# Kernel optimization log

Hardware: AMD Instinct MI355X
Metric: run time of the kernel (lower is better)

## Reference

```python
import jax, jax.numpy as jnp
import numpy as np

LSTM_H = 128
HID = 64
EMB = 64
GRU2_H = 50
B, T = 2048, 200
NODE_NUM = 50000


def _lstm_dir(x_proj, w_hh, reverse):
    # x_proj: (T, B, 4H) = x @ W_ih^T + b_ih + b_hh, precomputed
    Bn = x_proj.shape[1]
    H = w_hh.shape[1]
    h0 = jnp.zeros((Bn, H), x_proj.dtype)

    def step(carry, xp):
        h, c = carry
        gates = xp + h @ w_hh.T
        i, f, g, o = jnp.split(gates, 4, axis=-1)  # torch gate order i,f,g,o
        i = jax.nn.sigmoid(i); f = jax.nn.sigmoid(f)
        g = jnp.tanh(g); o = jax.nn.sigmoid(o)
        c = f * c + i * g
        h = o * jnp.tanh(c)
        return (h, c), h

    (hT, _), hs = jax.lax.scan(step, (h0, h0), x_proj, reverse=reverse)
    return hs, hT  # hs: (T,B,H) time-aligned; hT: final hidden of this direction


def _bilstm(x, wih_f, whh_f, b_f, wih_b, whh_b, b_b):
    # x: (B,T,I) batch_first -> scan over time
    xt = jnp.swapaxes(x, 0, 1)  # (T,B,I)
    hs_f, h_f = _lstm_dir(xt @ wih_f.T + b_f, whh_f, False)
    hs_b, h_b = _lstm_dir(xt @ wih_b.T + b_b, whh_b, True)
    out = jnp.concatenate([hs_f, hs_b], axis=-1)  # (T,B,2H)
    return jnp.swapaxes(out, 0, 1), jnp.stack([h_f, h_b])  # (B,T,2H), (2,B,H)


def _gru(x, h, wih, whh, bih, bhh):
    gi = x @ wih.T + bih
    gh = h @ whh.T + bhh
    ir, iz, inn = jnp.split(gi, 3, axis=-1)  # torch gate order r,z,n
    hr, hz, hn = jnp.split(gh, 3, axis=-1)
    r = jax.nn.sigmoid(ir + hr)
    z = jax.nn.sigmoid(iz + hz)
    n = jnp.tanh(inn + r * hn)
    return (1.0 - z) * n + z * h


def setup_inputs() -> dict:
    key = jax.random.key(0)
    ks = iter(jax.random.split(key, 40))
    s = 0.05
    d = {}
    d['node_data'] = jax.random.randint(next(ks), (B, 2), 0, NODE_NUM)
    d['edge_data'] = jax.random.uniform(next(ks), (B, T, 1), jnp.float32)
    d['emb'] = jax.random.normal(next(ks), (NODE_NUM, EMB), jnp.float32) * s
    # LSTM 1: input 1, hidden 128, bidirectional (b = b_ih + b_hh fused)
    d['l1_wih_f'] = jax.random.normal(next(ks), (4 * LSTM_H, 1), jnp.float32) * s
    d['l1_whh_f'] = jax.random.normal(next(ks), (4 * LSTM_H, LSTM_H), jnp.float32) * s
    d['l1_b_f'] = jax.random.normal(next(ks), (4 * LSTM_H,), jnp.float32) * s
    d['l1_wih_b'] = jax.random.normal(next(ks), (4 * LSTM_H, 1), jnp.float32) * s
    d['l1_whh_b'] = jax.random.normal(next(ks), (4 * LSTM_H, LSTM_H), jnp.float32) * s
    d['l1_b_b'] = jax.random.normal(next(ks), (4 * LSTM_H,), jnp.float32) * s
    # LSTM 2: input 256, hidden 128, bidirectional
    d['l2_wih_f'] = jax.random.normal(next(ks), (4 * LSTM_H, 2 * LSTM_H), jnp.float32) * s
    d['l2_whh_f'] = jax.random.normal(next(ks), (4 * LSTM_H, LSTM_H), jnp.float32) * s
    d['l2_b_f'] = jax.random.normal(next(ks), (4 * LSTM_H,), jnp.float32) * s
    d['l2_wih_b'] = jax.random.normal(next(ks), (4 * LSTM_H, 2 * LSTM_H), jnp.float32) * s
    d['l2_whh_b'] = jax.random.normal(next(ks), (4 * LSTM_H, LSTM_H), jnp.float32) * s
    d['l2_b_b'] = jax.random.normal(next(ks), (4 * LSTM_H,), jnp.float32) * s
    # encoder FCs
    d['fc1_w'] = jax.random.normal(next(ks), (2 * LSTM_H, 2 * LSTM_H), jnp.float32) * s
    d['fc1_b'] = jnp.zeros((2 * LSTM_H,), jnp.float32)
    d['fc2_w'] = jax.random.normal(next(ks), (HID, 2 * LSTM_H), jnp.float32) * s
    d['fc2_b'] = jnp.zeros((HID,), jnp.float32)
    # GRUCell 1: input 1, hidden HID+EMB=128
    G1 = HID + EMB
    d['g1_wih'] = jax.random.normal(next(ks), (3 * G1, 1), jnp.float32) * s
    d['g1_whh'] = jax.random.normal(next(ks), (3 * G1, G1), jnp.float32) * s
    d['g1_bih'] = jax.random.normal(next(ks), (3 * G1,), jnp.float32) * s
    d['g1_bhh'] = jax.random.normal(next(ks), (3 * G1,), jnp.float32) * s
    # GRUCell 2: input 128, hidden 50
    d['g2_wih'] = jax.random.normal(next(ks), (3 * GRU2_H, G1), jnp.float32) * s
    d['g2_whh'] = jax.random.normal(next(ks), (3 * GRU2_H, GRU2_H), jnp.float32) * s
    d['g2_bih'] = jax.random.normal(next(ks), (3 * GRU2_H,), jnp.float32) * s
    d['g2_bhh'] = jax.random.normal(next(ks), (3 * GRU2_H,), jnp.float32) * s
    # decoder FC: 50 -> 1
    d['dec_w'] = jax.random.normal(next(ks), (1, GRU2_H), jnp.float32) * s
    d['dec_b'] = jnp.zeros((1,), jnp.float32)
    return d


def reference(node_data, edge_data, emb,
              l1_wih_f, l1_whh_f, l1_b_f, l1_wih_b, l1_whh_b, l1_b_b,
              l2_wih_f, l2_whh_f, l2_b_f, l2_wih_b, l2_whh_b, l2_b_b,
              fc1_w, fc1_b, fc2_w, fc2_b,
              g1_wih, g1_whh, g1_bih, g1_bhh,
              g2_wih, g2_whh, g2_bih, g2_bhh,
              dec_w, dec_b):
    # ---- encoder ----
    node_embs = emb[node_data]                      # (B,2,EMB)
    node_emb = node_embs.mean(axis=1)               # (head+tail)/2
    h1_out, hn1 = _bilstm(edge_data, l1_wih_f, l1_whh_f, l1_b_f,
                          l1_wih_b, l1_whh_b, l1_b_b)
    _, hn2 = _bilstm(h1_out, l2_wih_f, l2_whh_f, l2_b_f,
                     l2_wih_b, l2_whh_b, l2_b_b)
    # faithful to original: view (2,B,128) -> (-1, 256) row-major (interleaves dir/batch)
    hidden_lstm = hn1.reshape(-1, 2 * LSTM_H) + hn2.reshape(-1, 2 * LSTM_H)
    h_fc1 = jax.nn.sigmoid(hidden_lstm @ fc1_w.T + fc1_b)  # dropout = identity (eval)
    temp_emb = jax.nn.sigmoid(h_fc1 @ fc2_w.T + fc2_b)
    hidden = jnp.concatenate([temp_emb, node_emb], axis=1)  # (B, HID+EMB)
    # ---- decoder: sequential GRU unroll as a scan ----
    Bn, max_len = edge_data.shape[0], edge_data.shape[1]
    h2_0 = jnp.zeros((Bn, GRU2_H), edge_data.dtype)

    def dstep(carry, _):
        res, h1, h2 = carry
        h1n = _gru(res, h1, g1_wih, g1_whh, g1_bih, g1_bhh)
        h2n = _gru(h1n, h2, g2_wih, g2_whh, g2_bih, g2_bhh)
        resn = jax.nn.sigmoid(h2n @ dec_w.T + dec_b)        # (B,1)
        return (resn, h1n, h2n), resn

    init = (edge_data[:, -1], hidden, h2_0)
    _, results = jax.lax.scan(dstep, init, None, length=max_len)
    return jnp.swapaxes(results, 0, 1)  # (B, max_len, 1)
```

## Files before the change

kernel.cpp:

```cpp
#include <hip/hip_runtime.h>
#include <stdint.h>

typedef short bf16x8 __attribute__((ext_vector_type(8)));
typedef float f32x4  __attribute__((ext_vector_type(4)));
typedef unsigned short u16;

#define NBATCH 2048
#define NT 200

#define MFMA_AG(accv, av, wfrag) \
  asm("v_mfma_f32_16x16x32_bf16 %0, %1, %2, %0" : "+v"(accv) : "v"(av), "a"(wfrag))
#define SEED_A(x) asm volatile("" : "+a"(x))
#define BAR() asm volatile("s_waitcnt lgkmcnt(0)\n\ts_barrier" ::: "memory")

#define OFF_HN1   209715200ull
#define OFF_HN2   211812352ull
#define OFF_ZC    213909504ull

__device__ __forceinline__ short f2bf(float f){
  union { float f; uint32_t u; } v; v.f = f;
  uint32_t u = v.u;
  u += 0x7fffu + ((u >> 16) & 1u);
  return (short)(u >> 16);
}
__device__ __forceinline__ float sigm(float x){
  return __builtin_amdgcn_rcpf(1.0f + __expf(-x));
}
__device__ __forceinline__ float tanh_(float x){
  return fmaf(-2.0f, __builtin_amdgcn_rcpf(1.0f + __expf(2.0f * x)), 1.0f);
}

__global__ void prep_l12(const float* __restrict__ l1hf, const float* __restrict__ l1hb,
                         const float* __restrict__ l2wf, const float* __restrict__ l2hf,
                         const float* __restrict__ l2wb, const float* __restrict__ l2hb,
                         u16* __restrict__ wl1, u16* __restrict__ wl2)
{
  int idx = blockIdx.x * 256 + threadIdx.x;
  if (idx < 16384){
    int tid = idx & 511, r = idx >> 9;
    int kt = r & 3, g = (r >> 2) & 3, d = r >> 4;
    const float* whh = d ? l1hb : l1hf;
    int wv = tid >> 6, ln = tid & 63, lr = ln & 15, lk = ln >> 4;
    int n = g * 128 + wv * 16 + lr;
    const float* s = whh + (size_t)n * 128 + kt * 32 + lk * 8;
    bf16x8 w;
#pragma unroll
    for (int i = 0; i < 8; ++i) w[i] = f2bf(s[i]);
    *(bf16x8*)(wl1 + (size_t)idx * 8) = w;
  } else {
    int j = idx - 16384;
    int tid = j & 511, r = j >> 9;
    int kt = r % 12, rg = r / 12;
    int g = rg & 3, d = rg >> 2;
    const float* wih = d ? l2wb : l2wf;
    const float* whh = d ? l2hb : l2hf;
    int wv = tid >> 6, ln = tid & 63, lr = ln & 15, lk = ln >> 4;
    int n = g * 128 + wv * 16 + lr;
    const float* s = (kt < 8) ? (wih + (size_t)n * 256 + kt * 32 + lk * 8)
                              : (whh + (size_t)n * 128 + (kt - 8) * 32 + lk * 8);
    bf16x8 w;
#pragma unroll
    for (int i = 0; i < 8; ++i) w[i] = f2bf(s[i]);
    *(bf16x8*)(wl2 + (size_t)j * 8) = w;
  }
}

__global__ void prep2(const float* __restrict__ g1whh, const float* __restrict__ g2wih,
                      const float* __restrict__ g2whh,
                      const float* __restrict__ fc1w, const float* __restrict__ fc2w,
                      const int* __restrict__ nd, const float* __restrict__ emb,
                      u16* __restrict__ wd1, u16* __restrict__ wd2i, u16* __restrict__ wd2h,
                      float* __restrict__ fc1wT, float* __restrict__ fc2wT,
                      float* __restrict__ ne)
{
  int idx = blockIdx.x * 256 + threadIdx.x;
  if (idx < 6144){
    int tid = idx & 511, r = idx >> 9;
    int kt = r & 3, g = r >> 2;
    int wv = tid >> 6, ln = tid & 63, lr = ln & 15, lk = ln >> 4;
    int n = g * 128 + wv * 16 + lr;
    const float* s = g1whh + (size_t)n * 128 + kt * 32 + lk * 8;
    bf16x8 w;
#pragma unroll
    for (int i = 0; i < 8; ++i) w[i] = f2bf(s[i]);
    *(bf16x8*)(wd1 + (size_t)idx * 8) = w;
  } else if (idx < 9216){
    int j = idx - 6144;
    int tid = j & 255, r = j >> 8;
    int kt = r & 3, g = r >> 2;
    int wv = tid >> 6, ln = tid & 63, lr = ln & 15, lk = ln >> 4;
    int jj = wv * 16 + lr;
    bf16x8 w;
#pragma unroll
    for (int i = 0; i < 8; ++i){
      int k = kt * 32 + lk * 8 + i;
      w[i] = (jj < 50) ? f2bf(g2wih[(size_t)(g * 50 + jj) * 128 + k]) : (short)0;
    }
    *(bf16x8*)(wd2i + (size_t)j * 8) = w;
  } else if (idx < 10752){
    int j = idx - 9216;
    int tid = j & 255, r = j >> 8;
    int kt = r & 1, g = r >> 1;
    int wv = tid >> 6, ln = tid & 63, lr = ln & 15, lk = ln >> 4;
    int jj = wv * 16 + lr;
    bf16x8 w;
#pragma unroll
    for (int i = 0; i < 8; ++i){
      int k = kt * 32 + lk * 8 + i;
      w[i] = (jj < 50 && k < 50) ? f2bf(g2whh[(size_t)(g * 50 + jj) * 50 + k]) : (short)0;
    }
    *(bf16x8*)(wd2h + (size_t)j * 8) = w;
  } else if (idx < 10752 + 65536){
    int j = idx - 10752;
    int n = j & 255, k = j >> 8;
    fc1wT[(size_t)k * 256 + n] = fc1w[(size_t)n * 256 + k];
  } else if (idx < 10752 + 81920){
    int j = idx - 10752 - 65536;
    int m = j & 63, k = j >> 6;
    fc2wT[(size_t)k * 64 + m] = fc2w[(size_t)m * 256 + k];
  } else {
    int t = idx - 92672;
    int row = t >> 6, e = t & 63;
    int i0 = nd[row * 2], i1 = nd[row * 2 + 1];
    ne[t] = 0.5f * (emb[(size_t)i0 * 64 + e] + emb[(size_t)i1 * 64 + e]);
  }
}

#define L1_KT(kt) { \
  int off = lr * 256 + (((kt) * 64 + lk * 16) ^ ((lr & 7) << 4)); \
  bf16x8 a = *(const bf16x8*)(hb + off); \
  MFMA_AG(acc[0], a, W[0][kt]); MFMA_AG(acc[1], a, W[1][kt]); \
  MFMA_AG(acc[2], a, W[2][kt]); MFMA_AG(acc[3], a, W[3][kt]); }

__global__ __launch_bounds__(512) __attribute__((amdgpu_waves_per_eu(2, 2))) void k_l1(
    const float* __restrict__ edge, const u16* __restrict__ wl1,
    const float* __restrict__ wih_f, const float* __restrict__ b_f,
    const float* __restrict__ wih_b, const float* __restrict__ b_b,
    u16* __restrict__ h1out, float* __restrict__ hn1)
{
  const int bid = blockIdx.x;
  const int dir = bid >> 7;
  const int b0  = (bid & 127) * 16;
  const float* wih = dir ? wih_b : wih_f;
  const float* bia = dir ? b_b  : b_f;

  const int tid = threadIdx.x;
  const int wv  = tid >> 6;
  const int ln  = tid & 63;
  const int lr  = ln & 15;
  const int lk  = ln >> 4;

  __shared__ __align__(16) short hbf[2][16 * 128];
  __shared__ float xall[16][NT];

  bf16x8 W[4][4];
  const u16* wb = wl1 + (size_t)dir * 16 * 512 * 8;
  float wv_[4], bv_[4];
#pragma unroll
  for (int g = 0; g < 4; ++g){
    int n = g * 128 + wv * 16 + lr;
    wv_[g] = wih[n];
    bv_[g] = bia[n];
#pragma unroll
    for (int kt = 0; kt < 4; ++kt){
      W[g][kt] = *(const bf16x8*)(wb + ((size_t)(g * 4 + kt) * 512 + tid) * 8);
      SEED_A(W[g][kt]);
    }
  }
  for (int i = tid; i < 16 * 128; i += 512) hbf[0][i] = 0;
  for (int i = tid; i < 16 * NT; i += 512){
    int r = i / NT, t = i - r * NT;
    xall[r][t] = edge[(b0 + r) * NT + t];
  }
  float cst[4] = {0.f, 0.f, 0.f, 0.f};
  float hseg[4] = {0.f, 0.f, 0.f, 0.f};
  __syncthreads();

  for (int s = 0; s < NT; ++s){
    const int p = s & 1;
    const int t = dir ? (NT - 1 - s) : s;

    const char* hb = (const char*)hbf + p * (16 * 256);
    f32x4 acc[4];
    float xq[4];
#pragma unroll
    for (int q = 0; q < 4; ++q) xq[q] = xall[lk * 4 + q][t];
#pragma unroll
    for (int g = 0; g < 4; ++g){
#pragma unroll
      for (int q = 0; q < 4; ++q) acc[g][q] = fmaf(xq[q], wv_[g], bv_[g]);
    }
    if (wv & 1){ L1_KT(2) L1_KT(3) L1_KT(0) L1_KT(1) }
    else       { L1_KT(0) L1_KT(1) L1_KT(2) L1_KT(3) }
    char* hbw = (char*)hbf + (p ^ 1) * (16 * 256);
#pragma unroll
    for (int q = 0; q < 4; ++q){
      float iv = sigm(acc[0][q]);
      float fv = sigm(acc[1][q]);
      float gv = tanh_(acc[2][q]);
      float ov = sigm(acc[3][q]);
      cst[q] = fv * cst[q] + iv * gv;
      hseg[q] = ov * tanh_(cst[q]);
      short hv = f2bf(hseg[q]);
      int r = lk * 4 + q, j = wv * 16 + lr;
      h1out[((size_t)t * NBATCH + b0 + r) * 256 + dir * 128 + j] = (u16)hv;
      *(short*)(hbw + r * 256 + ((2 * j) ^ ((r & 7) << 4))) = hv;
    }
    BAR();
  }
#pragma unroll
  for (int q = 0; q < 4; ++q)
    hn1[((size_t)dir * NBATCH + b0 + lk * 4 + q) * 128 + wv * 16 + lr] = hseg[q];
}

#define L2_LDSKT(kt) { \
  int off = lr * 768 + (((kt) * 64 + lk * 16) ^ ((lr & 7) << 4)); \
  bf16x8 a = *(const bf16x8*)(ab + off); \
  bf16x8 w0 = *(const bf16x8*)&wlds[((size_t)(0 * 4 + (kt)) * 512 + tid) * 8]; \
  acc[0] = __builtin_amdgcn_mfma_f32_16x16x32_bf16(a, w0, acc[0], 0, 0, 0); \
  bf16x8 w1 = *(const bf16x8*)&wlds[((size_t)(1 * 4 + (kt)) * 512 + tid) * 8]; \
  acc[1] = __builtin_amdgcn_mfma_f32_16x16x32_bf16(a, w1, acc[1], 0, 0, 0); \
  bf16x8 w2 = *(const bf16x8*)&wlds[((size_t)(2 * 4 + (kt)) * 512 + tid) * 8]; \
  acc[2] = __builtin_amdgcn_mfma_f32_16x16x32_bf16(a, w2, acc[2], 0, 0, 0); \
  bf16x8 w3 = *(const bf16x8*)&wlds[((size_t)(3 * 4 + (kt)) * 512 + tid) * 8]; \
  acc[3] = __builtin_amdgcn_mfma_f32_16x16x32_bf16(a, w3, acc[3], 0, 0, 0); }

#define L2_AGKT(k8) { \
  int off = lr * 768 + (((4 + (k8)) * 64 + lk * 16) ^ ((lr & 7) << 4)); \
  bf16x8 a = *(const bf16x8*)(ab + off); \
  MFMA_AG(acc[0], a, Wa[0][k8]); MFMA_AG(acc[1], a, Wa[1][k8]); \
  MFMA_AG(acc[2], a, Wa[2][k8]); MFMA_AG(acc[3], a, Wa[3][k8]); }

__global__ __launch_bounds__(512) __attribute__((amdgpu_waves_per_eu(2, 2))) void k_l2(
    const u16* __restrict__ h1out, const u16* __restrict__ wl2,
    const float* __restrict__ b_f, const float* __restrict__ b_b,
    float* __restrict__ hn2)
{
  const int bid = blockIdx.x;
  const int dir = bid >> 7;
  const int b0  = (bid & 127) * 16;
  const float* bia = dir ? b_b : b_f;

  const int tid = threadIdx.x;
  const int wv  = tid >> 6;
  const int ln  = tid & 63;
  const int lr  = ln & 15;
  const int lk  = ln >> 4;

  __shared__ __align__(16) short wlds[16 * 512 * 8];
  __shared__ __align__(16) short Ab[2][16 * 384];

  const u16* wb = wl2 + (size_t)dir * 48 * 512 * 8;
#pragma unroll
  for (int f = 0; f < 16; ++f){
    int g = f >> 2, kt = f & 3;
    *(bf16x8*)&wlds[((size_t)f * 512 + tid) * 8] =
        *(const bf16x8*)(wb + ((size_t)(g * 12 + kt) * 512 + tid) * 8);
  }
  bf16x8 Wa[4][8];
  float bv_[4];
#pragma unroll
  for (int g = 0; g < 4; ++g){
    bv_[g] = bia[g * 128 + wv * 16 + lr];
#pragma unroll
    for (int k8 = 0; k8 < 8; ++k8){
      Wa[g][k8] = *(const bf16x8*)(wb + ((size_t)(g * 12 + 4 + k8) * 512 + tid) * 8);
      SEED_A(Wa[g][k8]);
    }
  }
  for (int i = tid; i < 16 * 128; i += 512){
    int r = i >> 7, j = i & 127;
    *(short*)((char*)Ab + r * 768 + ((512 + 2 * j) ^ ((r & 7) << 4))) = 0;
  }
  const int sr = tid >> 5, sg = tid & 31;
  {
    int t0 = dir ? NT - 1 : 0;
    bf16x8 v = *(const bf16x8*)(h1out + ((size_t)t0 * NBATCH + b0 + sr) * 256 + sg * 8);
    *(bf16x8*)((char*)Ab + sr * 768 + ((sg * 16) ^ ((sr & 7) << 4))) = v;
  }
  float cst[4] = {0.f, 0.f, 0.f, 0.f};
  float hseg[4] = {0.f, 0.f, 0.f, 0.f};
  __syncthreads();

  for (int s = 0; s < NT; ++s){
    const int p = s & 1;
    const int t = dir ? (NT - 1 - s) : s;
    const int tn = dir ? (t > 0 ? t - 1 : 0) : (t < NT - 1 ? t + 1 : NT - 1);
    bf16x8 xr = *(const bf16x8*)(h1out + ((size_t)tn * NBATCH + b0 + sr) * 256 + sg * 8);

    const char* ab = (const char*)Ab + p * (16 * 768);
    f32x4 acc[4];
#pragma unroll
    for (int g = 0; g < 4; ++g){
#pragma unroll
      for (int q = 0; q < 4; ++q) acc[g][q] = bv_[g];
    }
    if (wv & 1){
      L2_AGKT(0) L2_AGKT(1) L2_AGKT(2) L2_AGKT(3)
      L2_AGKT(4) L2_AGKT(5) L2_AGKT(6) L2_AGKT(7)
      L2_LDSKT(0) L2_LDSKT(1) L2_LDSKT(2) L2_LDSKT(3)
    } else {
      L2_LDSKT(0) L2_LDSKT(1) L2_LDSKT(2) L2_LDSKT(3)
      L2_AGKT(0) L2_AGKT(1) L2_AGKT(2) L2_AGKT(3)
      L2_AGKT(4) L2_AGKT(5) L2_AGKT(6) L2_AGKT(7)
    }
    char* abw = (char*)Ab + (p ^ 1) * (16 * 768);
#pragma unroll
    for (int q = 0; q < 4; ++q){
      float iv = sigm(acc[0][q]);
      float fv = sigm(acc[1][q]);
      float gv = tanh_(acc[2][q]);
      float ov = sigm(acc[3][q]);
      cst[q] = fv * cst[q] + iv * gv;
      hseg[q] = ov * tanh_(cst[q]);
      int r = lk * 4 + q, j = wv * 16 + lr;
      *(short*)(abw + r * 768 + ((512 + 2 * j) ^ ((r & 7) << 4))) = f2bf(hseg[q]);
    }
    *(bf16x8*)(abw + sr * 768 + ((sg * 16) ^ ((sr & 7) << 4))) = xr;
    BAR();
  }
#pragma unroll
  for (int q = 0; q < 4; ++q)
    hn2[((size_t)dir * NBATCH + b0 + lk * 4 + q) * 128 + wv * 16 + lr] = hseg[q];
}

__global__ __launch_bounds__(256) void k_fc(
    const float* __restrict__ hn1, const float* __restrict__ hn2,
    const float* __restrict__ fc1wT, const float* __restrict__ fc1b,
    const float* __restrict__ fc2wT, const float* __restrict__ fc2b,
    const float* __restrict__ ne, float* __restrict__ hidden)
{
  __shared__ float X[16][256];
  __shared__ float Y[16][256];
  const int b0 = blockIdx.x * 16;
  const int tid = threadIdx.x;
  for (int i = tid; i < 16 * 256; i += 256){
    int rr = i >> 8, cc = i & 255;
    size_t o = (size_t)(b0 + rr) * 256 + cc;
    X[rr][cc] = hn1[o] + hn2[o];
  }
  __syncthreads();
  {
    const int n = tid;
    float a[16];
#pragma unroll
    for (int r = 0; r < 16; ++r) a[r] = fc1b[n];
    for (int k = 0; k < 256; ++k){
      float w = fc1wT[(size_t)k * 256 + n];
#pragma unroll
      for (int r = 0; r < 16; ++r) a[r] = fmaf(X[r][k], w, a[r]);
    }
#pragma unroll
    for (int r = 0; r < 16; ++r) Y[r][n] = sigm(a[r]);
  }
  __syncthreads();
  {
    const int m = tid & 63, rg = tid >> 6;
    float a2[4];
#pragma unroll
    for (int q = 0; q < 4; ++q) a2[q] = fc2b[m];
    for (int k = 0; k < 256; ++k){
      float w = fc2wT[(size_t)k * 64 + m];
#pragma unroll
      for (int q = 0; q < 4; ++q) a2[q] = fmaf(Y[rg * 4 + q][k], w, a2[q]);
    }
#pragma unroll
    for (int q = 0; q < 4; ++q)
      hidden[(size_t)(b0 + rg * 4 + q) * 128 + m] = sigm(a2[q]);
  }
  for (int i = tid; i < 16 * 64; i += 256){
    int rr = i >> 6, e = i & 63;
    hidden[(size_t)(b0 + rr) * 128 + 64 + e] = ne[(size_t)(b0 + rr) * 64 + e];
  }
}

#define D1_KT(kt) { \
  int off = lr * 256 + (((kt) * 64 + lk * 16) ^ ((lr & 7) << 4)); \
  bf16x8 a = *(const bf16x8*)(h1r + off); \
  MFMA_AG(ar, a, W1[0][kt]); MFMA_AG(az, a, W1[1][kt]); MFMA_AG(an, a, W1[2][kt]); }

#define D2_KT(kt) { \
  int off = lr * 256 + (((kt) * 64 + lk * 16) ^ ((lr & 7) << 4)); \
  bf16x8 a = *(const bf16x8*)(h1n + off); \
  MFMA_AG(gi0, a, Wi2[0][kt]); MFMA_AG(gi1, a, Wi2[1][kt]); MFMA_AG(gi2v, a, Wi2[2][kt]); }

__global__ __launch_bounds__(512) __attribute__((amdgpu_waves_per_eu(2, 2))) void k_dec(
    const float* __restrict__ edge, const float* __restrict__ hidden,
    const float* __restrict__ g1wih, const float* __restrict__ g1bih,
    const float* __restrict__ g1bhh, const u16* __restrict__ wd1,
    const float* __restrict__ g2bih, const float* __restrict__ g2bhh,
    const u16* __restrict__ wd2i, const u16* __restrict__ wd2h,
    const float* __restrict__ decw, const float* __restrict__ decb,
    float* __restrict__ out)
{
  const int b0 = blockIdx.x * 16;
  const int tid = threadIdx.x;
  const int wv  = tid >> 6;
  const int ln  = tid & 63;
  const int lr  = ln & 15;
  const int lk  = ln >> 4;

  __shared__ __align__(16) short h1bf[2][16 * 128];
  __shared__ __align__(16) short h2bf[2][16 * 64];
  __shared__ float part[2][4][16];

  bf16x8 W1[3][4];
  float wih1v[3], bih1v[3], bhh1v[3];
#pragma unroll
  for (int g = 0; g < 3; ++g){
    int n = g * 128 + wv * 16 + lr;
    wih1v[g] = g1wih[n];
    bih1v[g] = g1bih[n];
    bhh1v[g] = g1bhh[n];
#pragma unroll
    for (int kt = 0; kt < 4; ++kt){
      W1[g][kt] = *(const bf16x8*)(wd1 + ((size_t)(g * 4 + kt) * 512 + tid) * 8);
      SEED_A(W1[g][kt]);
    }
  }
  bf16x8 Wi2[3][4], Wh2[3][2];
  float bih2v[3] = {0,0,0}, bhh2v[3] = {0,0,0}, dwv = 0.f;
  const int jj = wv * 16 + lr;
  if (wv < 4){
    bool nv_ = (jj < 50);
    dwv = nv_ ? decw[jj] : 0.f;
#pragma unroll
    for (int g = 0; g < 3; ++g){
      bih2v[g] = nv_ ? g2bih[g * 50 + jj] : 0.f;
      bhh2v[g] = nv_ ? g2bhh[g * 50 + jj] : 0.f;
#pragma unroll
      for (int kt = 0; kt < 4; ++kt){
        Wi2[g][kt] = *(const bf16x8*)(wd2i + ((size_t)(g * 4 + kt) * 256 + tid) * 8);
        SEED_A(Wi2[g][kt]);
      }
#pragma unroll
      for (int kt = 0; kt < 2; ++kt){
        Wh2[g][kt] = *(const bf16x8*)(wd2h + ((size_t)(g * 2 + kt) * 256 + tid) * 8);
        SEED_A(Wh2[g][kt]);
      }
    }
  }
  float h1s[4], h2s[4] = {0.f, 0.f, 0.f, 0.f}, e4[4];
#pragma unroll
  for (int q = 0; q < 4; ++q){
    h1s[q] = hidden[(size_t)(b0 + lk * 4 + q) * 128 + wv * 16 + lr];
    int r = lk * 4 + q, j = wv * 16 + lr;
    *(short*)((char*)h1bf + r * 256 + ((2 * j) ^ ((r & 7) << 4))) = f2bf(h1s[q]);
    e4[q] = edge[(b0 + r) * NT + NT - 1];
  }
  for (int i = tid; i < 16 * 64; i += 512) h2bf[0][i] = 0;
  const float db = decb[0];
  __syncthreads();

  for (int s = 0; s < NT; ++s){
    const int p = s & 1;
    float res_q[4];
    if (s == 0){
#pragma unroll
      for (int q = 0; q < 4; ++q) res_q[q] = e4[q];
    } else {
#pragma unroll
      for (int q = 0; q < 4; ++q){
        int row = lk * 4 + q;
        float sum = part[p][0][row] + part[p][1][row] + part[p][2][row] + part[p][3][row] + db;
        res_q[q] = sigm(sum);
        if (wv == 0 && lr == 0) out[(size_t)(b0 + row) * NT + (s - 1)] = res_q[q];
      }
    }
    const char* h1r = (const char*)h1bf + p * (16 * 256);
    f32x4 ar, az, an;
#pragma unroll
    for (int q = 0; q < 4; ++q){ ar[q] = bhh1v[0]; az[q] = bhh1v[1]; an[q] = bhh1v[2]; }
    if (wv & 1){ D1_KT(2) D1_KT(3) D1_KT(0) D1_KT(1) }
    else       { D1_KT(0) D1_KT(1) D1_KT(2) D1_KT(3) }
    char* h1w = (char*)h1bf + (p ^ 1) * (16 * 256);
#pragma unroll
    for (int q = 0; q < 4; ++q){
      float res = res_q[q];
      float rv = sigm(fmaf(res, wih1v[0], bih1v[0]) + ar[q]);
      float zv = sigm(fmaf(res, wih1v[1], bih1v[1]) + az[q]);
      float nv = tanh_(fmaf(res, wih1v[2], bih1v[2]) + rv * an[q]);
      h1s[q] = (1.f - zv) * nv + zv * h1s[q];
      int r = lk * 4 + q, j = wv * 16 + lr;
      *(short*)(h1w + r * 256 + ((2 * j) ^ ((r & 7) << 4))) = f2bf(h1s[q]);
    }
    BAR();
    if (wv < 4){
      f32x4 gi0, gi1, gi2v, gh0, gh1, gh2v;
#pragma unroll
      for (int q = 0; q < 4; ++q){
        gi0[q] = bih2v[0]; gi1[q] = bih2v[1]; gi2v[q] = bih2v[2];
        gh0[q] = bhh2v[0]; gh1[q] = bhh2v[1]; gh2v[q] = bhh2v[2];
      }
      const char* h1n = (const char*)h1bf + (p ^ 1) * (16 * 256);
      if (wv & 1){ D2_KT(2) D2_KT(3) D2_KT(0) D2_KT(1) }
      else       { D2_KT(0) D2_KT(1) D2_KT(2) D2_KT(3) }
      const char* h2r = (const char*)h2bf + p * (16 * 128);
#pragma unroll
      for (int kt = 0; kt < 2; ++kt){
        int off = lr * 128 + ((kt * 64 + lk * 16) ^ ((lr & 7) << 4));
        bf16x8 a = *(const bf16x8*)(h2r + off);
        MFMA_AG(gh0,  a, Wh2[0][kt]);
        MFMA_AG(gh1,  a, Wh2[1][kt]);
        MFMA_AG(gh2v, a, Wh2[2][kt]);
      }
      char* h2w = (char*)h2bf + (p ^ 1) * (16 * 128);
      float pd[4];
#pragma unroll
      for (int q = 0; q < 4; ++q){
        float r2 = sigm(gi0[q] + gh0[q]);
        float z2 = sigm(gi1[q] + gh1[q]);
        float n2 = tanh_(gi2v[q] + r2 * gh2v[q]);
        h2s[q] = (1.f - z2) * n2 + z2 * h2s[q];
        pd[q] = h2s[q] * dwv;
        int r = lk * 4 + q, j = wv * 16 + lr;
        *(short*)(h2w + r * 128 + ((2 * j) ^ ((r & 7) << 4))) = f2bf(h2s[q]);
      }
#pragma unroll
      for (int m = 1; m < 16; m <<= 1){
#pragma unroll
        for (int q = 0; q < 4; ++q) pd[q] += __shfl_xor(pd[q], m);
      }
      if (lr == 0){
#pragma unroll
        for (int q = 0; q < 4; ++q) part[p ^ 1][wv][lk * 4 + q] = pd[q];
      }
    }
    BAR();
  }
  if (wv == 0 && lr == 0){
#pragma unroll
    for (int q = 0; q < 4; ++q){
      int row = lk * 4 + q;
      float sum = part[0][0][row] + part[0][1][row] + part[0][2][row] + part[0][3][row] + db;
      out[(size_t)(b0 + row) * NT + (NT - 1)] = sigm(sum);
    }
  }
}

extern "C" void kernel_launch(void* const* d_in, const int* in_sizes, int n_in,
                              void* d_out, int out_size, void* d_ws, size_t ws_size,
                              hipStream_t stream)
{
  (void)in_sizes; (void)n_in; (void)out_size; (void)ws_size;
  const int*   nd    = (const int*)  d_in[0];
  const float* edge  = (const float*)d_in[1];
  const float* emb   = (const float*)d_in[2];
  const float* l1wf  = (const float*)d_in[3];
  const float* l1hf  = (const float*)d_in[4];
  const float* l1bf  = (const float*)d_in[5];
  const float* l1wb  = (const float*)d_in[6];
  const float* l1hb  = (const float*)d_in[7];
  const float* l1bb  = (const float*)d_in[8];
  const float* l2wf  = (const float*)d_in[9];
  const float* l2hf  = (const float*)d_in[10];
  const float* l2bf  = (const float*)d_in[11];
  const float* l2wb  = (const float*)d_in[12];
  const float* l2hb  = (const float*)d_in[13];
  const float* l2bb  = (const float*)d_in[14];
  const float* fc1w  = (const float*)d_in[15];
  const float* fc1b  = (const float*)d_in[16];
  const float* fc2w  = (const float*)d_in[17];
  const float* fc2b  = (const float*)d_in[18];
  const float* g1wih = (const float*)d_in[19];
  const float* g1whh = (const float*)d_in[20];
  const float* g1bih = (const float*)d_in[21];
  const float* g1bhh = (const float*)d_in[22];
  const float* g2wih = (const float*)d_in[23];
  const float* g2whh = (const float*)d_in[24];
  const float* g2bih = (const float*)d_in[25];
  const float* g2bhh = (const float*)d_in[26];
  const float* decw  = (const float*)d_in[27];
  const float* decb  = (const float*)d_in[28];

  char* ws = (char*)d_ws;
  u16*   h1out  = (u16*)ws;
  u16*   wd1    = (u16*)ws;
  u16*   wd2i   = (u16*)(ws + 98304);
  u16*   wd2h   = (u16*)(ws + 147456);
  float* fc1wT  = (float*)(ws + 262144);
  float* fc2wT  = (float*)(ws + 524288);
  float* hn1    = (float*)(ws + OFF_HN1);
  float* hn2    = (float*)(ws + OFF_HN2);
  u16*   wl2    = (u16*)(ws + OFF_ZC);
  u16*   wl1    = (u16*)(ws + OFF_ZC + 786432);
  float* ne     = (float*)(ws + OFF_ZC);
  float* hidden = (float*)(ws + OFF_ZC + 524288);

  prep_l12<<<dim3(256), dim3(256), 0, stream>>>(l1hf, l1hb, l2wf, l2hf, l2wb, l2hb, wl1, wl2);
  k_l1<<<dim3(256), dim3(512), 0, stream>>>(edge, wl1, l1wf, l1bf, l1wb, l1bb, h1out, hn1);
  k_l2<<<dim3(256), dim3(512), 0, stream>>>(h1out, wl2, l2bf, l2bb, hn2);
  prep2<<<dim3(874), dim3(256), 0, stream>>>(g1whh, g2wih, g2whh, fc1w, fc2w, nd, emb,
                                             wd1, wd2i, wd2h, fc1wT, fc2wT, ne);
  k_fc<<<dim3(128), dim3(256), 0, stream>>>(hn1, hn2, fc1wT, fc1b, fc2wT, fc2b, ne, hidden);
  k_dec<<<dim3(128), dim3(512), 0, stream>>>(edge, hidden, g1wih, g1bih, g1bhh, wd1,
                                             g2bih, g2bhh, wd2i, wd2h, decw, decb,
                                             (float*)d_out);
}
```

Before: 1.046 ms.

## Split LSTM1 into 8-row blocks and software-pipeline LSTM2 input projection

Layer-1 LSTM now runs 512 blocks of 256 threads, each handling 8 batch rows with every wave computing two 16-column tiles per gate. The MFMA uses only half of its 16 rows; the other half are duplicates. This spreads the serial recurrence over more CUs at the price of doing the MFMA work twice. Layer-2 now keeps the input-projection buffer separate from the hidden-state buffer, and computes the input part for the next step before the current step's gate nonlinearities, so that part falls outside the serial h dependency chain. The register-held weights move to the Wx and Wh halves, and the split of weights between registers and LDS changes with them.

```diff
diff --git a/kernel.cpp b/kernel.cpp
--- a/kernel.cpp
+++ b/kernel.cpp
@@ -37,11 +37,11 @@
 {
   int idx = blockIdx.x * 256 + threadIdx.x;
   if (idx < 16384){
-    int tid = idx & 511, r = idx >> 9;
-    int kt = r & 3, g = (r >> 2) & 3, d = r >> 4;
+    int tid = idx & 255, r = idx >> 8;
+    int kt = r & 3, u = (r >> 2) & 1, g = (r >> 3) & 3, d = r >> 5;
     const float* whh = d ? l1hb : l1hf;
     int wv = tid >> 6, ln = tid & 63, lr = ln & 15, lk = ln >> 4;
-    int n = g * 128 + wv * 16 + lr;
+    int n = g * 128 + wv * 32 + u * 16 + lr;
     const float* s = whh + (size_t)n * 128 + kt * 32 + lk * 8;
     bf16x8 w;
 #pragma unroll
@@ -126,21 +126,15 @@
   }
 }
 
-#define L1_KT(kt) { \
-  int off = lr * 256 + (((kt) * 64 + lk * 16) ^ ((lr & 7) << 4)); \
-  bf16x8 a = *(const bf16x8*)(hb + off); \
-  MFMA_AG(acc[0], a, W[0][kt]); MFMA_AG(acc[1], a, W[1][kt]); \
-  MFMA_AG(acc[2], a, W[2][kt]); MFMA_AG(acc[3], a, W[3][kt]); }
-
-__global__ __launch_bounds__(512) __attribute__((amdgpu_waves_per_eu(2, 2))) void k_l1(
+__global__ __launch_bounds__(256) __attribute__((amdgpu_waves_per_eu(2, 2))) void k_l1(
     const float* __restrict__ edge, const u16* __restrict__ wl1,
     const float* __restrict__ wih_f, const float* __restrict__ b_f,
     const float* __restrict__ wih_b, const float* __restrict__ b_b,
     u16* __restrict__ h1out, float* __restrict__ hn1)
 {
   const int bid = blockIdx.x;
-  const int dir = bid >> 7;
-  const int b0  = (bid & 127) * 16;
+  const int dir = bid >> 8;
+  const int b0  = (bid & 255) * 8;
   const float* wih = dir ? wih_b : wih_f;
   const float* bia = dir ? b_b  : b_f;
 
@@ -151,29 +145,31 @@
   const int lk  = ln >> 4;
 
   __shared__ __align__(16) short hbf[2][16 * 128];
-  __shared__ float xall[16][NT];
-
-  bf16x8 W[4][4];
-  const u16* wb = wl1 + (size_t)dir * 16 * 512 * 8;
-  float wv_[4], bv_[4];
-#pragma unroll
-  for (int g = 0; g < 4; ++g){
-    int n = g * 128 + wv * 16 + lr;
-    wv_[g] = wih[n];
-    bv_[g] = bia[n];
-#pragma unroll
-    for (int kt = 0; kt < 4; ++kt){
-      W[g][kt] = *(const bf16x8*)(wb + ((size_t)(g * 4 + kt) * 512 + tid) * 8);
-      SEED_A(W[g][kt]);
-    }
-  }
-  for (int i = tid; i < 16 * 128; i += 512) hbf[0][i] = 0;
-  for (int i = tid; i < 16 * NT; i += 512){
+  __shared__ float xall[8][NT];
+
+  bf16x8 W[4][2][4];
+  const u16* wb = wl1 + (size_t)dir * 32 * 256 * 8;
+  float wv_[4][2], bv_[4][2];
+#pragma unroll
+  for (int g = 0; g < 4; ++g)
+#pragma unroll
+    for (int u = 0; u < 2; ++u){
+      int n = g * 128 + wv * 32 + u * 16 + lr;
+      wv_[g][u] = wih[n];
+      bv_[g][u] = bia[n];
+#pragma unroll
+      for (int kt = 0; kt < 4; ++kt){
+        W[g][u][kt] = *(const bf16x8*)(wb + ((size_t)((g * 8 + u * 4 + kt)) * 256 + tid) * 8);
+        SEED_A(W[g][u][kt]);
+      }
+    }
+  for (int i = tid; i < 16 * 128; i += 256) hbf[0][i] = 0;
+  for (int i = tid; i < 8 * NT; i += 256){
     int r = i / NT, t = i - r * NT;
     xall[r][t] = edge[(b0 + r) * NT + t];
   }
-  float cst[4] = {0.f, 0.f, 0.f, 0.f};
-  float hseg[4] = {0.f, 0.f, 0.f, 0.f};
+  float cst[2][4] = {{0,0,0,0},{0,0,0,0}};
+  float hseg[2][4] = {{0,0,0,0},{0,0,0,0}};
   __syncthreads();
 
   for (int s = 0; s < NT; ++s){
@@ -181,55 +177,53 @@
     const int t = dir ? (NT - 1 - s) : s;
 
     const char* hb = (const char*)hbf + p * (16 * 256);
-    f32x4 acc[4];
+    f32x4 acc[4][2];
     float xq[4];
 #pragma unroll
-    for (int q = 0; q < 4; ++q) xq[q] = xall[lk * 4 + q][t];
-#pragma unroll
-    for (int g = 0; g < 4; ++g){
-#pragma unroll
-      for (int q = 0; q < 4; ++q) acc[g][q] = fmaf(xq[q], wv_[g], bv_[g]);
-    }
-    if (wv & 1){ L1_KT(2) L1_KT(3) L1_KT(0) L1_KT(1) }
-    else       { L1_KT(0) L1_KT(1) L1_KT(2) L1_KT(3) }
+    for (int q = 0; q < 4; ++q) xq[q] = xall[(lk * 4 + q) & 7][t];
+#pragma unroll
+    for (int g = 0; g < 4; ++g)
+#pragma unroll
+      for (int u = 0; u < 2; ++u)
+#pragma unroll
+        for (int q = 0; q < 4; ++q) acc[g][u][q] = fmaf(xq[q], wv_[g][u], bv_[g][u]);
+#pragma unroll
+    for (int kt = 0; kt < 4; ++kt){
+      int off = lr * 256 + ((kt * 64 + lk * 16) ^ ((lr & 7) << 4));
+      bf16x8 a = *(const bf16x8*)(hb + off);
+#pragma unroll
+      for (int g = 0; g < 4; ++g)
+#pragma unroll
+        for (int u = 0; u < 2; ++u) MFMA_AG(acc[g][u], a, W[g][u][kt]);
+    }
     char* hbw = (char*)hbf + (p ^ 1) * (16 * 256);
 #pragma unroll
+    for (int u = 0; u < 2; ++u)
+#pragma unroll
+      for (int q = 0; q < 4; ++q){
+        float iv = sigm(acc[0][u][q]);
+        float fv = sigm(acc[1][u][q]);
+        float gv = tanh_(acc[2][u][q]);
+        float ov = sigm(acc[3][u][q]);
+        cst[u][q] = fv * cst[u][q] + iv * gv;
+        hseg[u][q] = ov * tanh_(cst[u][q]);
+        short hv = f2bf(hseg[u][q]);
+        int r = lk * 4 + q, j = wv * 32 + u * 16 + lr;
+        if (r < 8)
+          h1out[((size_t)t * NBATCH + b0 + r) * 256 + dir * 128 + j] = (u16)hv;
+        *(short*)(hbw + r * 256 + ((2 * j) ^ ((r & 7) << 4))) = hv;
+      }
+    BAR();
+  }
+#pragma unroll
+  for (int u = 0; u < 2; ++u)
+#pragma unroll
     for (int q = 0; q < 4; ++q){
-      float iv = sigm(acc[0][q]);
-      float fv = sigm(acc[1][q]);
-      float gv = tanh_(acc[2][q]);
-      float ov = sigm(acc[3][q]);
-      cst[q] = fv * cst[q] + iv * gv;
-      hseg[q] = ov * tanh_(cst[q]);
-      short hv = f2bf(hseg[q]);
-      int r = lk * 4 + q, j = wv * 16 + lr;
-      h1out[((size_t)t * NBATCH + b0 + r) * 256 + dir * 128 + j] = (u16)hv;
-      *(short*)(hbw + r * 256 + ((2 * j) ^ ((r & 7) << 4))) = hv;
-    }
-    BAR();
-  }
-#pragma unroll
-  for (int q = 0; q < 4; ++q)
-    hn1[((size_t)dir * NBATCH + b0 + lk * 4 + q) * 128 + wv * 16 + lr] = hseg[q];
-}
-
-#define L2_LDSKT(kt) { \
-  int off = lr * 768 + (((kt) * 64 + lk * 16) ^ ((lr & 7) << 4)); \
-  bf16x8 a = *(const bf16x8*)(ab + off); \
-  bf16x8 w0 = *(const bf16x8*)&wlds[((size_t)(0 * 4 + (kt)) * 512 + tid) * 8]; \
-  acc[0] = __builtin_amdgcn_mfma_f32_16x16x32_bf16(a, w0, acc[0], 0, 0, 0); \
-  bf16x8 w1 = *(const bf16x8*)&wlds[((size_t)(1 * 4 + (kt)) * 512 + tid) * 8]; \
-  acc[1] = __builtin_amdgcn_mfma_f32_16x16x32_bf16(a, w1, acc[1], 0, 0, 0); \
-  bf16x8 w2 = *(const bf16x8*)&wlds[((size_t)(2 * 4 + (kt)) * 512 + tid) * 8]; \
-  acc[2] = __builtin_amdgcn_mfma_f32_16x16x32_bf16(a, w2, acc[2], 0, 0, 0); \
-  bf16x8 w3 = *(const bf16x8*)&wlds[((size_t)(3 * 4 + (kt)) * 512 + tid) * 8]; \
-  acc[3] = __builtin_amdgcn_mfma_f32_16x16x32_bf16(a, w3, acc[3], 0, 0, 0); }
-
-#define L2_AGKT(k8) { \
-  int off = lr * 768 + (((4 + (k8)) * 64 + lk * 16) ^ ((lr & 7) << 4)); \
-  bf16x8 a = *(const bf16x8*)(ab + off); \
-  MFMA_AG(acc[0], a, Wa[0][k8]); MFMA_AG(acc[1], a, Wa[1][k8]); \
-  MFMA_AG(acc[2], a, Wa[2][k8]); MFMA_AG(acc[3], a, Wa[3][k8]); }
+      int r = lk * 4 + q;
+      if (r < 8)
+        hn1[((size_t)dir * NBATCH + b0 + r) * 128 + wv * 32 + u * 16 + lr] = hseg[u][q];
+    }
+}
 
 __global__ __launch_bounds__(512) __attribute__((amdgpu_waves_per_eu(2, 2))) void k_l2(
     const u16* __restrict__ h1out, const u16* __restrict__ wl2,
@@ -248,63 +242,77 @@
   const int lk  = ln >> 4;
 
   __shared__ __align__(16) short wlds[16 * 512 * 8];
-  __shared__ __align__(16) short Ab[2][16 * 384];
+  __shared__ __align__(16) short Xb[2][16 * 256];
+  __shared__ __align__(16) short Hb[2][16 * 128];
 
   const u16* wb = wl2 + (size_t)dir * 48 * 512 * 8;
 #pragma unroll
   for (int f = 0; f < 16; ++f){
-    int g = f >> 2, kt = f & 3;
+    int g = f >> 2, kx = f & 3;
     *(bf16x8*)&wlds[((size_t)f * 512 + tid) * 8] =
-        *(const bf16x8*)(wb + ((size_t)(g * 12 + kt) * 512 + tid) * 8);
-  }
-  bf16x8 Wa[4][8];
+        *(const bf16x8*)(wb + ((size_t)(g * 12 + 4 + kx) * 512 + tid) * 8);
+  }
+  bf16x8 Wx[4][4], Wh[4][4];
   float bv_[4];
 #pragma unroll
   for (int g = 0; g < 4; ++g){
     bv_[g] = bia[g * 128 + wv * 16 + lr];
 #pragma unroll
-    for (int k8 = 0; k8 < 8; ++k8){
-      Wa[g][k8] = *(const bf16x8*)(wb + ((size_t)(g * 12 + 4 + k8) * 512 + tid) * 8);
-      SEED_A(Wa[g][k8]);
+    for (int k = 0; k < 4; ++k){
+      Wx[g][k] = *(const bf16x8*)(wb + ((size_t)(g * 12 + k) * 512 + tid) * 8);
+      SEED_A(Wx[g][k]);
+      Wh[g][k] = *(const bf16x8*)(wb + ((size_t)(g * 12 + 8 + k) * 512 + tid) * 8);
+      SEED_A(Wh[g][k]);
     }
   }
   for (int i = tid; i < 16 * 128; i += 512){
     int r = i >> 7, j = i & 127;
-    *(short*)((char*)Ab + r * 768 + ((512 + 2 * j) ^ ((r & 7) << 4))) = 0;
+    *(short*)((char*)Hb + r * 256 + ((2 * j) ^ ((r & 7) << 4))) = 0;
   }
   const int sr = tid >> 5, sg = tid & 31;
-  {
-    int t0 = dir ? NT - 1 : 0;
-    bf16x8 v = *(const bf16x8*)(h1out + ((size_t)t0 * NBATCH + b0 + sr) * 256 + sg * 8);
-    *(bf16x8*)((char*)Ab + sr * 768 + ((sg * 16) ^ ((sr & 7) << 4))) = v;
-  }
+  auto XLD = [&](int k) -> bf16x8 {
+    int kk = k < NT ? k : NT - 1;
+    int t = dir ? (NT - 1 - kk) : kk;
+    return *(const bf16x8*)(h1out + ((size_t)t * NBATCH + b0 + sr) * 256 + sg * 8);
+  };
+  auto XST = [&](char* xb, bf16x8 v){
+    *(bf16x8*)(xb + sr * 512 + ((sg * 16) ^ ((sr & 7) << 4))) = v;
+  };
+  XST((char*)Xb[0], XLD(0));
+  XST((char*)Xb[1], XLD(1));
   float cst[4] = {0.f, 0.f, 0.f, 0.f};
   float hseg[4] = {0.f, 0.f, 0.f, 0.f};
   __syncthreads();
 
-  for (int s = 0; s < NT; ++s){
-    const int p = s & 1;
-    const int t = dir ? (NT - 1 - s) : s;
-    const int tn = dir ? (t > 0 ? t - 1 : 0) : (t < NT - 1 ? t + 1 : NT - 1);
-    bf16x8 xr = *(const bf16x8*)(h1out + ((size_t)tn * NBATCH + b0 + sr) * 256 + sg * 8);
-
-    const char* ab = (const char*)Ab + p * (16 * 768);
-    f32x4 acc[4];
-#pragma unroll
-    for (int g = 0; g < 4; ++g){
-#pragma unroll
-      for (int q = 0; q < 4; ++q) acc[g][q] = bv_[g];
-    }
-    if (wv & 1){
-      L2_AGKT(0) L2_AGKT(1) L2_AGKT(2) L2_AGKT(3)
-      L2_AGKT(4) L2_AGKT(5) L2_AGKT(6) L2_AGKT(7)
-      L2_LDSKT(0) L2_LDSKT(1) L2_LDSKT(2) L2_LDSKT(3)
-    } else {
-      L2_LDSKT(0) L2_LDSKT(1) L2_LDSKT(2) L2_LDSKT(3)
-      L2_AGKT(0) L2_AGKT(1) L2_AGKT(2) L2_AGKT(3)
-      L2_AGKT(4) L2_AGKT(5) L2_AGKT(6) L2_AGKT(7)
-    }
-    char* abw = (char*)Ab + (p ^ 1) * (16 * 768);
+  auto HPART = [&](f32x4* acc, const char* hb){
+#pragma unroll
+    for (int k = 0; k < 4; ++k){
+      int off = lr * 256 + ((k * 64 + lk * 16) ^ ((lr & 7) << 4));
+      bf16x8 a = *(const bf16x8*)(hb + off);
+      MFMA_AG(acc[0], a, Wh[0][k]); MFMA_AG(acc[1], a, Wh[1][k]);
+      MFMA_AG(acc[2], a, Wh[2][k]); MFMA_AG(acc[3], a, Wh[3][k]);
+    }
+  };
+  auto XPART = [&](f32x4* acc, const char* xb){
+#pragma unroll
+    for (int k = 0; k < 4; ++k){
+      int off = lr * 512 + ((k * 64 + lk * 16) ^ ((lr & 7) << 4));
+      bf16x8 a = *(const bf16x8*)(xb + off);
+      MFMA_AG(acc[0], a, Wx[0][k]); MFMA_AG(acc[1], a, Wx[1][k]);
+      MFMA_AG(acc[2], a, Wx[2][k]); MFMA_AG(acc[3], a, Wx[3][k]);
+    }
+#pragma unroll
+    for (int k = 0; k < 4; ++k){
+      int off = lr * 512 + (((4 + k) * 64 + lk * 16) ^ ((lr & 7) << 4));
+      bf16x8 a = *(const bf16x8*)(xb + off);
+#pragma unroll
+      for (int g = 0; g < 4; ++g){
+        bf16x8 w = *(const bf16x8*)&wlds[((size_t)(g * 4 + k) * 512 + tid) * 8];
+        acc[g] = __builtin_amdgcn_mfma_f32_16x16x32_bf16(a, w, acc[g], 0, 0, 0);
+      }
+    }
+  };
+  auto GATES = [&](f32x4* acc, char* hbw){
 #pragma unroll
     for (int q = 0; q < 4; ++q){
       float iv = sigm(acc[0][q]);
@@ -314,9 +322,39 @@
       cst[q] = fv * cst[q] + iv * gv;
       hseg[q] = ov * tanh_(cst[q]);
       int r = lk * 4 + q, j = wv * 16 + lr;
-      *(short*)(abw + r * 768 + ((512 + 2 * j) ^ ((r & 7) << 4))) = f2bf(hseg[q]);
-    }
-    *(bf16x8*)(abw + sr * 768 + ((sg * 16) ^ ((sr & 7) << 4))) = xr;
+      *(short*)(hbw + r * 256 + ((2 * j) ^ ((r & 7) << 4))) = f2bf(hseg[q]);
+    }
+  };
+
+  f32x4 accA[4], accB[4];
+#pragma unroll
+  for (int g = 0; g < 4; ++g)
+#pragma unroll
+    for (int q = 0; q < 4; ++q) accA[g][q] = bv_[g];
+  XPART(accA, (const char*)Xb[0]);
+  bf16x8 xr = XLD(2);
+  BAR();
+
+  for (int s = 0; s < NT; s += 2){
+    HPART(accA, (const char*)Hb[0]);
+#pragma unroll
+    for (int g = 0; g < 4; ++g)
+#pragma unroll
+      for (int q = 0; q < 4; ++q) accB[g][q] = bv_[g];
+    XPART(accB, (const char*)Xb[1]);
+    GATES(accA, (char*)Hb[1]);
+    XST((char*)Xb[0], xr);
+    xr = XLD(s + 3);
+    BAR();
+    HPART(accB, (const char*)Hb[1]);
+#pragma unroll
+    for (int g = 0; g < 4; ++g)
+#pragma unroll
+      for (int q = 0; q < 4; ++q) accA[g][q] = bv_[g];
+    XPART(accA, (const char*)Xb[0]);
+    GATES(accB, (char*)Hb[0]);
+    XST((char*)Xb[1], xr);
+    xr = XLD(s + 4);
     BAR();
   }
 #pragma unroll
@@ -588,7 +626,7 @@
   float* hidden = (float*)(ws + OFF_ZC + 524288);
 
   prep_l12<<<dim3(256), dim3(256), 0, stream>>>(l1hf, l1hb, l2wf, l2hf, l2wb, l2hb, wl1, wl2);
-  k_l1<<<dim3(256), dim3(512), 0, stream>>>(edge, wl1, l1wf, l1bf, l1wb, l1bb, h1out, hn1);
+  k_l1<<<dim3(512), dim3(256), 0, stream>>>(edge, wl1, l1wf, l1bf, l1wb, l1bb, h1out, hn1);
   k_l2<<<dim3(256), dim3(512), 0, stream>>>(h1out, wl2, l2bf, l2bb, hn2);
   prep2<<<dim3(874), dim3(256), 0, stream>>>(g1whh, g2wih, g2whh, fc1w, fc2w, nd, emb,
                                              wd1, wd2i, wd2h, fc1wT, fc2wT, ne);
```

New measurement: 1.528 ms. +46.1%, slower.
